# Optimization experiments

Measured on AMD Instinct MI355X. Metric: run time of the kernel, lower is better.

## Reference

```python
import jax, jax.numpy as jnp
import numpy as np

N_GENES = 20000   # num_all_genes
D = 256           # embedding_dim
NNZ = 640000      # nonzeros in GO adjacency (~32 avg degree)
N_COND = 2000     # number of conditions
B = 16384         # batch size
MAXG = 5          # max_genes_per_condition
L = 2             # num_gnn_layers


def setup_inputs() -> dict:
    key = jax.random.key(0)
    ks = jax.random.split(key, 12)
    cond_idx = jax.random.randint(ks[0], (B,), 0, N_COND, dtype=jnp.int32)
    pert_embedding = jax.random.normal(ks[1], (N_GENES, D), jnp.float32) * 0.05
    gnn_kernels = jax.random.normal(ks[2], (L, D, D), jnp.float32) * 0.05
    mlp_w1 = jax.random.normal(ks[3], (D, D), jnp.float32) * 0.05
    mlp_b1 = jnp.zeros((D,), jnp.float32)
    mlp_w2 = jax.random.normal(ks[4], (D, D), jnp.float32) * 0.05
    mlp_b2 = jnp.zeros((D,), jnp.float32)
    adj_row = jax.random.randint(ks[5], (NNZ,), 0, N_GENES, dtype=jnp.int64)
    adj_col = jax.random.randint(ks[6], (NNZ,), 0, N_GENES, dtype=jnp.int64)
    adj_vals = jax.random.uniform(ks[7], (NNZ,), jnp.float32)
    cond_gene_idx = jax.random.randint(ks[8], (N_COND, MAXG), 0, N_GENES, dtype=jnp.int32)
    counts = jax.random.randint(ks[9], (N_COND,), 0, MAXG + 1)
    cond_gene_mask = (jnp.arange(MAXG)[None, :] < counts[:, None]).astype(jnp.float32)
    # padded slots get -1 index like the original (later clamped to 0)
    cond_gene_idx = jnp.where(cond_gene_mask > 0, cond_gene_idx, -1)
    return {
        'cond_idx': cond_idx,
        'pert_embedding': pert_embedding,
        'gnn_kernels': gnn_kernels,
        'mlp_w1': mlp_w1, 'mlp_b1': mlp_b1,
        'mlp_w2': mlp_w2, 'mlp_b2': mlp_b2,
        'adj_row': adj_row, 'adj_col': adj_col, 'adj_vals': adj_vals,
        'cond_gene_idx': cond_gene_idx, 'cond_gene_mask': cond_gene_mask,
    }


def reference(cond_idx, pert_embedding, gnn_kernels, mlp_w1, mlp_b1,
              mlp_w2, mlp_b2, adj_row, adj_col, adj_vals,
              cond_gene_idx, cond_gene_mask):
    # --- GNN over the full gene graph (sparse adjacency @ dense emb, then dense kernel) ---
    emb = pert_embedding  # [N, D]
    for i in range(L):
        # SpMM: aggregated[r] = sum_{nnz with row r} vals * emb[col]
        msgs = adj_vals[:, None] * emb[adj_col]            # [NNZ, D]
        agg = jax.ops.segment_sum(msgs, adj_row, num_segments=N_GENES)  # [N, D]
        emb = agg @ gnn_kernels[i]                          # [N, D]
        if i < L - 1:
            emb = jax.nn.relu(emb)

    # --- per-condition gather of up to MAXG gene embeddings, masked sum ---
    gidx = cond_gene_idx[cond_idx]          # [B, MAXG] int
    gmask = cond_gene_mask[cond_idx]        # [B, MAXG]
    gidx_safe = jnp.maximum(gidx, 0)
    gene_embs = emb[gidx_safe]              # [B, MAXG, D]
    summed = jnp.sum(gene_embs * gmask[:, :, None], axis=1)  # [B, D]
    n_genes = jnp.sum(gmask, axis=1)        # [B]

    # --- small MLP (applied when n_genes > 1), identity when ==1, zeros when ==0 ---
    h = jax.nn.relu(summed @ mlp_w1 + mlp_b1)
    mlp_out = jax.nn.relu(h @ mlp_w2 + mlp_b2)  # [B, D]

    n = n_genes[:, None]
    out = jnp.where(n == 0.0, 0.0, jnp.where(n == 1.0, summed, mlp_out))
    return out
```

## Files before the change

### kernel.cpp

```cpp
#include <hip/hip_runtime.h>

static constexpr int N_GENES = 20000;
static constexpr int D       = 256;
static constexpr int NNZ     = 640000;
static constexpr int BATCH   = 16384;
static constexpr int MAXG    = 5;
static constexpr int SCAN_B  = (N_GENES + 255) / 256;

using bf16x8 = __attribute__((ext_vector_type(8))) short;
using f32x4  = __attribute__((ext_vector_type(4))) float;

__device__ __forceinline__ unsigned short f2bf(float f) {
  unsigned int u = __builtin_bit_cast(unsigned int, f);
  u += 0x7fffu + ((u >> 16) & 1u);
  return (unsigned short)(u >> 16);
}
__device__ __forceinline__ float bf2f(unsigned short h) {
  unsigned int u = ((unsigned int)h) << 16;
  return __builtin_bit_cast(float, u);
}
__device__ __forceinline__ void gload16(const void* g, void* l) {
  __builtin_amdgcn_global_load_lds(
      (const __attribute__((address_space(1))) unsigned int*)g,
      (__attribute__((address_space(3))) unsigned int*)l, 16, 0, 0);
}

__global__ void zero_int(int* __restrict__ p, int n) {
  int i = blockIdx.x * blockDim.x + threadIdx.x;
  if (i < n) p[i] = 0;
}

__global__ void count_rows(const int* __restrict__ adj_row, int* __restrict__ cnt) {
  int e = blockIdx.x * blockDim.x + threadIdx.x;
  if (e < NNZ) atomicAdd(&cnt[adj_row[e]], 1);
}

__global__ __launch_bounds__(256)
void scan_partial(const int* __restrict__ cnt, int* __restrict__ bsum) {
  __shared__ int red[256];
  int b = blockIdx.x, t = threadIdx.x, i = b * 256 + t;
  red[t] = (i < N_GENES) ? cnt[i] : 0;
  __syncthreads();
  for (int off = 128; off > 0; off >>= 1) {
    if (t < off) red[t] += red[t + off];
    __syncthreads();
  }
  if (t == 0) bsum[b] = red[0];
}

__global__ __launch_bounds__(128)
void scan_bsums(const int* __restrict__ bsum, int* __restrict__ bpre,
                int* __restrict__ total_out) {
  __shared__ int s[128];
  int t = threadIdx.x;
  int x = (t < SCAN_B) ? bsum[t] : 0;
  s[t] = x;
  __syncthreads();
  for (int off = 1; off < 128; off <<= 1) {
    int v = (t >= off) ? s[t - off] : 0;
    __syncthreads();
    s[t] += v;
    __syncthreads();
  }
  if (t < SCAN_B) bpre[t] = s[t] - x;
  if (t == SCAN_B - 1) total_out[0] = s[t];
}

__global__ __launch_bounds__(256)
void scan_final(const int* __restrict__ cnt, const int* __restrict__ bpre,
                int* __restrict__ row_ptr, int* __restrict__ fill_ctr) {
  __shared__ int s[256];
  int b = blockIdx.x, t = threadIdx.x, i = b * 256 + t;
  int x = (i < N_GENES) ? cnt[i] : 0;
  s[t] = x;
  __syncthreads();
  for (int off = 1; off < 256; off <<= 1) {
    int v = (t >= off) ? s[t - off] : 0;
    __syncthreads();
    s[t] += v;
    __syncthreads();
  }
  if (i < N_GENES) {
    int e = bpre[b] + s[t] - x;
    row_ptr[i] = e;
    fill_ctr[i] = e;
  }
}

__global__ void fill_csr(const int* __restrict__ adj_row,
                         const int* __restrict__ adj_col,
                         const float* __restrict__ vals,
                         int* __restrict__ fill_ctr, unsigned int* __restrict__ edges) {
  int e = blockIdx.x * blockDim.x + threadIdx.x;
  if (e < NNZ) {
    int r = adj_row[e];
    int p = atomicAdd(&fill_ctr[r], 1);
    edges[p] = (unsigned int)adj_col[e] | ((unsigned int)f2bf(vals[e]) << 16);
  }
}

__global__ __launch_bounds__(256)
void conv_pert(const float* __restrict__ p, ushort4* __restrict__ o) {
  int i = blockIdx.x * 256 + threadIdx.x;
  float4 v = reinterpret_cast<const float4*>(p)[i];
  ushort4 r;
  r.x = f2bf(v.x); r.y = f2bf(v.y); r.z = f2bf(v.z); r.w = f2bf(v.w);
  o[i] = r;
}

__global__ void conv_weights(const float* __restrict__ gk, const float* __restrict__ w1,
                             const float* __restrict__ w2,
                             char* __restrict__ whi, char* __restrict__ wlo) {
  int g = blockIdx.x * 256 + threadIdx.x;
  int wid = g >> 13, rest = g & 8191;
  const float* W = (wid == 0) ? gk : (wid == 1) ? gk + 65536 : (wid == 2) ? w1 : w2;
  int c  = rest >> 9;
  int nc = c >> 2, kt = c & 3;
  int o  = (rest & 511) << 4;
  int n  = o >> 7;
  int wb = (o & 127) ^ ((n & 7) << 4);
  int k  = wb >> 1;
  size_t obase = ((size_t)wid << 17) + ((size_t)c << 13) + o;
  unsigned short* ph = (unsigned short*)(whi + obase);
  unsigned short* pl = (unsigned short*)(wlo + obase);
  #pragma unroll
  for (int e = 0; e < 8; ++e) {
    float f = W[(size_t)(kt * 64 + k + e) * 256 + nc * 64 + n];
    unsigned short h = f2bf(f);
    ph[e] = h;
    pl[e] = f2bf(f - bf2f(h));
  }
}

__global__ __launch_bounds__(256)
void spmm_csr_img(const int* __restrict__ row_ptr, const unsigned int* __restrict__ edges,
                  const unsigned short* __restrict__ src,
                  char* __restrict__ hi_img, char* __restrict__ lo_img) {
  int row = blockIdx.x * 4 + (threadIdx.x >> 6);
  int lane = threadIdx.x & 63;
  int beg = row_ptr[row], end = row_ptr[row + 1];
  const unsigned short* sp = src + lane * 4;
  float4 acc = {0.f, 0.f, 0.f, 0.f};
  int j = beg;
  for (; j + 8 <= end; j += 8) {
    unsigned int e0 = edges[j],     e1 = edges[j + 1], e2 = edges[j + 2], e3 = edges[j + 3];
    unsigned int e4 = edges[j + 4], e5 = edges[j + 5], e6 = edges[j + 6], e7 = edges[j + 7];
    ushort4 g0 = *reinterpret_cast<const ushort4*>(sp + (size_t)(e0 & 0xFFFFu) * D);
    ushort4 g1 = *reinterpret_cast<const ushort4*>(sp + (size_t)(e1 & 0xFFFFu) * D);
    ushort4 g2 = *reinterpret_cast<const ushort4*>(sp + (size_t)(e2 & 0xFFFFu) * D);
    ushort4 g3 = *reinterpret_cast<const ushort4*>(sp + (size_t)(e3 & 0xFFFFu) * D);
    ushort4 g4 = *reinterpret_cast<const ushort4*>(sp + (size_t)(e4 & 0xFFFFu) * D);
    ushort4 g5 = *reinterpret_cast<const ushort4*>(sp + (size_t)(e5 & 0xFFFFu) * D);
    ushort4 g6 = *reinterpret_cast<const ushort4*>(sp + (size_t)(e6 & 0xFFFFu) * D);
    ushort4 g7 = *reinterpret_cast<const ushort4*>(sp + (size_t)(e7 & 0xFFFFu) * D);
    float v0 = bf2f(e0 >> 16), v1 = bf2f(e1 >> 16), v2 = bf2f(e2 >> 16), v3 = bf2f(e3 >> 16);
    float v4 = bf2f(e4 >> 16), v5 = bf2f(e5 >> 16), v6 = bf2f(e6 >> 16), v7 = bf2f(e7 >> 16);
    acc.x += v0 * bf2f(g0.x); acc.y += v0 * bf2f(g0.y); acc.z += v0 * bf2f(g0.z); acc.w += v0 * bf2f(g0.w);
    acc.x += v1 * bf2f(g1.x); acc.y += v1 * bf2f(g1.y); acc.z += v1 * bf2f(g1.z); acc.w += v1 * bf2f(g1.w);
    acc.x += v2 * bf2f(g2.x); acc.y += v2 * bf2f(g2.y); acc.z += v2 * bf2f(g2.z); acc.w += v2 * bf2f(g2.w);
    acc.x += v3 * bf2f(g3.x); acc.y += v3 * bf2f(g3.y); acc.z += v3 * bf2f(g3.z); acc.w += v3 * bf2f(g3.w);
    acc.x += v4 * bf2f(g4.x); acc.y += v4 * bf2f(g4.y); acc.z += v4 * bf2f(g4.z); acc.w += v4 * bf2f(g4.w);
    acc.x += v5 * bf2f(g5.x); acc.y += v5 * bf2f(g5.y); acc.z += v5 * bf2f(g5.z); acc.w += v5 * bf2f(g5.w);
    acc.x += v6 * bf2f(g6.x); acc.y += v6 * bf2f(g6.y); acc.z += v6 * bf2f(g6.z); acc.w += v6 * bf2f(g6.w);
    acc.x += v7 * bf2f(g7.x); acc.y += v7 * bf2f(g7.y); acc.z += v7 * bf2f(g7.z); acc.w += v7 * bf2f(g7.w);
  }
  for (; j < end; ++j) {
    unsigned int e = edges[j];
    ushort4 g = *reinterpret_cast<const ushort4*>(sp + (size_t)(e & 0xFFFFu) * D);
    float v = bf2f(e >> 16);
    acc.x += v * bf2f(g.x); acc.y += v * bf2f(g.y); acc.z += v * bf2f(g.z); acc.w += v * bf2f(g.w);
  }
  int mt = row >> 7, r = row & 127, kt = lane >> 4;
  int wb = ((lane & 15) << 3) ^ ((r & 7) << 4);
  size_t off = ((size_t)(mt * 4 + kt) << 14) + (size_t)r * 128 + wb;
  float a4[4] = {acc.x, acc.y, acc.z, acc.w};
  ushort4 hi, lo;
  unsigned short* ph = (unsigned short*)&hi;
  unsigned short* pl = (unsigned short*)&lo;
  #pragma unroll
  for (int e = 0; e < 4; ++e) {
    unsigned short h = f2bf(a4[e]);
    ph[e] = h;
    pl[e] = f2bf(a4[e] - bf2f(h));
  }
  *reinterpret_cast<ushort4*>(hi_img + off) = hi;
  *reinterpret_cast<ushort4*>(lo_img + off) = lo;
}

__global__ __launch_bounds__(256)
void gather_conditions(const int* __restrict__ cond_idx, const int* __restrict__ cg_idx,
                       const float* __restrict__ cg_mask, const float* __restrict__ emb,
                       float* __restrict__ out, char* __restrict__ hi_img,
                       char* __restrict__ lo_img, float* __restrict__ ngenes) {
  int b = blockIdx.x * 4 + (threadIdx.x >> 6);
  int lane = threadIdx.x & 63;
  int c = cond_idx[b];
  float4 acc = {0.f, 0.f, 0.f, 0.f};
  float n = 0.f;
  #pragma unroll
  for (int g = 0; g < MAXG; ++g) {
    float m = cg_mask[c * MAXG + g];
    n += m;
    if (m > 0.f) {
      int gi = cg_idx[c * MAXG + g];
      float4 e = *reinterpret_cast<const float4*>(emb + (size_t)gi * D + lane * 4);
      acc.x += m * e.x; acc.y += m * e.y; acc.z += m * e.z; acc.w += m * e.w;
    }
  }
  *reinterpret_cast<float4*>(out + (size_t)b * D + lane * 4) = acc;
  int mt = b >> 7, r = b & 127, kt = lane >> 4;
  int wb = ((lane & 15) << 3) ^ ((r & 7) << 4);
  size_t off = ((size_t)(mt * 4 + kt) << 14) + (size_t)r * 128 + wb;
  float a4[4] = {acc.x, acc.y, acc.z, acc.w};
  ushort4 hi, lo;
  unsigned short* ph = (unsigned short*)&hi;
  unsigned short* pl = (unsigned short*)&lo;
  #pragma unroll
  for (int e = 0; e < 4; ++e) {
    unsigned short h = f2bf(a4[e]);
    ph[e] = h;
    pl[e] = f2bf(a4[e] - bf2f(h));
  }
  *reinterpret_cast<ushort4*>(hi_img + off) = hi;
  *reinterpret_cast<ushort4*>(lo_img + off) = lo;
  if (lane == 0) ngenes[b] = n;
}

enum Epi { E_F32, E_RELU_BF16, E_HIMG, E_SELECT };

template <Epi EP>
__global__ __launch_bounds__(256)
void gemm_bf16x3(const char* __restrict__ Ahi, const char* __restrict__ Alo,
                 const char* __restrict__ Bhi, const char* __restrict__ Blo,
                 const float* __restrict__ bias, float* __restrict__ C,
                 unsigned short* __restrict__ Cbf,
                 char* __restrict__ Ohi, char* __restrict__ Olo,
                 const float* __restrict__ ngenes, int M) {
  __shared__ __align__(16) char smem[65536];
  char* sAh = smem;
  char* sAl = smem + 16384;
  char* sBh = smem + 32768;
  char* sBl = smem + 49152;

  const int t   = threadIdx.x;
  const int w   = t >> 6, l = t & 63;
  const int wr  = w >> 1, wc = w & 1;
  const int mt  = blockIdx.y, nt2 = blockIdx.x;

  f32x4 acc[4][4] = {};

  const int rA = l & 15;
  const int kB = (l >> 4) << 4;
  const int xA = (rA & 7) << 4;

  for (int kt = 0; kt < 4; ++kt) {
    const char* gAh  = Ahi + ((size_t)(mt * 4 + kt) << 14);
    const char* gAl  = Alo + ((size_t)(mt * 4 + kt) << 14);
    const char* gBh0 = Bhi + ((size_t)((nt2 * 2 + 0) * 4 + kt) << 13);
    const char* gBl0 = Blo + ((size_t)((nt2 * 2 + 0) * 4 + kt) << 13);
    const char* gBh1 = Bhi + ((size_t)((nt2 * 2 + 1) * 4 + kt) << 13);
    const char* gBl1 = Blo + ((size_t)((nt2 * 2 + 1) * 4 + kt) << 13);
    #pragma unroll
    for (int j = 0; j < 4; ++j) {
      gload16(gAh + (j * 256 + t) * 16, sAh + j * 4096 + w * 1024);
      gload16(gAl + (j * 256 + t) * 16, sAl + j * 4096 + w * 1024);
    }
    #pragma unroll
    for (int j = 0; j < 2; ++j) {
      gload16(gBh0 + (j * 256 + t) * 16, sBh + j * 4096 + w * 1024);
      gload16(gBl0 + (j * 256 + t) * 16, sBl + j * 4096 + w * 1024);
    }
    #pragma unroll
    for (int j = 0; j < 2; ++j) {
      gload16(gBh1 + (j * 256 + t) * 16, sBh + 8192 + j * 4096 + w * 1024);
      gload16(gBl1 + (j * 256 + t) * 16, sBl + 8192 + j * 4096 + w * 1024);
    }
    asm volatile("s_waitcnt vmcnt(0)" ::: "memory");
    __syncthreads();
    #pragma unroll
    for (int ks = 0; ks < 2; ++ks) {
      bf16x8 ah[4], al[4], bh[4], bl[4];
      #pragma unroll
      for (int i = 0; i < 4; ++i) {
        int r   = wr * 64 + i * 16 + rA;
        int off = r * 128 + ((ks * 64 + kB) ^ xA);
        ah[i] = *(const bf16x8*)(sAh + off);
        al[i] = *(const bf16x8*)(sAl + off);
      }
      #pragma unroll
      for (int j = 0; j < 4; ++j) {
        int n   = wc * 64 + j * 16 + rA;
        int off = n * 128 + ((ks * 64 + kB) ^ xA);
        bh[j] = *(const bf16x8*)(sBh + off);
        bl[j] = *(const bf16x8*)(sBl + off);
      }
      #pragma unroll
      for (int i = 0; i < 4; ++i)
        #pragma unroll
        for (int j = 0; j < 4; ++j) {
          acc[i][j] = __builtin_amdgcn_mfma_f32_16x16x32_bf16(ah[i], bh[j], acc[i][j], 0, 0, 0);
          acc[i][j] = __builtin_amdgcn_mfma_f32_16x16x32_bf16(ah[i], bl[j], acc[i][j], 0, 0, 0);
          acc[i][j] = __builtin_amdgcn_mfma_f32_16x16x32_bf16(al[i], bh[j], acc[i][j], 0, 0, 0);
        }
    }
    __syncthreads();
  }

  const int cr = (l >> 4) << 2;
  const int cc = l & 15;
  #pragma unroll
  for (int i = 0; i < 4; ++i) {
    #pragma unroll
    for (int rr = 0; rr < 4; ++rr) {
      int rin  = wr * 64 + i * 16 + cr + rr;
      int grow = mt * 128 + rin;
      if (grow >= M) continue;
      bool wr_row = true;
      if (EP == E_SELECT) wr_row = (ngenes[grow] >= 1.5f);
      #pragma unroll
      for (int j = 0; j < 4; ++j) {
        float v    = acc[i][j][rr];
        int colin  = wc * 64 + j * 16 + cc;
        int gcol   = nt2 * 128 + colin;
        if (EP == E_HIMG || EP == E_SELECT) v += bias[gcol];
        if (EP != E_F32) v = fmaxf(v, 0.f);
        if (EP == E_HIMG) {
          int kt2 = nt2 * 2 + (colin >> 6);
          int k2  = colin & 63;
          int wb  = (k2 << 1) ^ ((rin & 7) << 4);
          size_t off = ((size_t)(mt * 4 + kt2) << 14) + (size_t)rin * 128 + wb;
          unsigned short h16 = f2bf(v);
          *(unsigned short*)(Ohi + off) = h16;
          *(unsigned short*)(Olo + off) = f2bf(v - bf2f(h16));
        } else if (EP == E_RELU_BF16) {
          Cbf[(size_t)grow * 256 + gcol] = f2bf(v);
        } else if (wr_row) {
          C[(size_t)grow * 256 + gcol] = v;
        }
      }
    }
  }
}

extern "C" void kernel_launch(void* const* d_in, const int* in_sizes, int n_in,
                              void* d_out, int out_size, void* d_ws, size_t ws_size,
                              hipStream_t stream) {
  const int*   cond_idx = (const int*)d_in[0];
  const float* pert     = (const float*)d_in[1];
  const float* gnn_k    = (const float*)d_in[2];
  const float* w1       = (const float*)d_in[3];
  const float* b1       = (const float*)d_in[4];
  const float* w2       = (const float*)d_in[5];
  const float* b2       = (const float*)d_in[6];
  const int*   adj_row  = (const int*)d_in[7];
  const int*   adj_col  = (const int*)d_in[8];
  const float* adj_vals = (const float*)d_in[9];
  const int*   cg_idx   = (const int*)d_in[10];
  const float* cg_mask  = (const float*)d_in[11];
  float* out = (float*)d_out;

  char* w = (char*)d_ws;
  auto alloc = [&](size_t bytes) {
    void* p = w;
    w += (bytes + 255) & ~size_t(255);
    return p;
  };
  constexpr int MT_G = (N_GENES + 127) / 128;
  constexpr int MT_B = BATCH / 128;
  char*         aggHi   = (char*)alloc((size_t)MT_G * 4 * 16384);
  char*         aggLo   = (char*)alloc((size_t)MT_G * 4 * 16384);
  float*        embf    = (float*)alloc((size_t)N_GENES * D * 4);
  char*         sumHi   = (char*)alloc((size_t)MT_B * 4 * 16384);
  char*         sumLo   = (char*)alloc((size_t)MT_B * 4 * 16384);
  char*         hHi     = (char*)alloc((size_t)MT_B * 4 * 16384);
  char*         hLo     = (char*)alloc((size_t)MT_B * 4 * 16384);
  char*         wHi     = (char*)alloc((size_t)4 << 17);
  char*         wLo     = (char*)alloc((size_t)4 << 17);
  unsigned int* edges   = (unsigned int*)alloc((size_t)NNZ * 4);
  int*          cnt     = (int*)alloc((size_t)N_GENES * 4);
  int*          row_ptr = (int*)alloc((size_t)(N_GENES + 4) * 4);
  int*          fill_ctr= (int*)alloc((size_t)N_GENES * 4);
  int*          bsum    = (int*)alloc((size_t)128 * 4);
  int*          bpre    = (int*)alloc((size_t)128 * 4);
  float*        ngenes  = (float*)alloc((size_t)BATCH * 4);

  unsigned short* pert_bf = (unsigned short*)hHi;
  unsigned short* embf_bf = (unsigned short*)embf;

  zero_int<<<(N_GENES + 255) / 256, 256, 0, stream>>>(cnt, N_GENES);
  count_rows<<<NNZ / 256, 256, 0, stream>>>(adj_row, cnt);
  scan_partial<<<SCAN_B, 256, 0, stream>>>(cnt, bsum);
  scan_bsums<<<1, 128, 0, stream>>>(bsum, bpre, row_ptr + N_GENES);
  scan_final<<<SCAN_B, 256, 0, stream>>>(cnt, bpre, row_ptr, fill_ctr);
  fill_csr<<<NNZ / 256, 256, 0, stream>>>(adj_row, adj_col, adj_vals, fill_ctr, edges);

  conv_weights<<<128, 256, 0, stream>>>(gnn_k, w1, w2, wHi, wLo);
  conv_pert<<<N_GENES * D / 4 / 256, 256, 0, stream>>>(pert, (ushort4*)pert_bf);

  spmm_csr_img<<<N_GENES / 4, 256, 0, stream>>>(row_ptr, edges, pert_bf, aggHi, aggLo);
  gemm_bf16x3<E_RELU_BF16><<<dim3(2, MT_G), 256, 0, stream>>>(
      aggHi, aggLo, wHi, wLo, nullptr, nullptr, embf_bf, nullptr, nullptr, nullptr, N_GENES);

  spmm_csr_img<<<N_GENES / 4, 256, 0, stream>>>(row_ptr, edges, embf_bf, aggHi, aggLo);
  gemm_bf16x3<E_F32><<<dim3(2, MT_G), 256, 0, stream>>>(
      aggHi, aggLo, wHi + (1 << 17), wLo + (1 << 17), nullptr, embf, nullptr, nullptr, nullptr, nullptr, N_GENES);

  gather_conditions<<<BATCH / 4, 256, 0, stream>>>(cond_idx, cg_idx, cg_mask, embf,
                                                   out, sumHi, sumLo, ngenes);

  gemm_bf16x3<E_HIMG><<<dim3(2, MT_B), 256, 0, stream>>>(
      sumHi, sumLo, wHi + (2 << 17), wLo + (2 << 17), b1, nullptr, nullptr, hHi, hLo, nullptr, BATCH);

  gemm_bf16x3<E_SELECT><<<dim3(2, MT_B), 256, 0, stream>>>(
      hHi, hLo, wHi + (3 << 17), wLo + (3 << 17), b2, out, nullptr, nullptr, nullptr, ngenes, BATCH);
}
```

Measured before the change: 329.9 us.

## Fuse CSR fill and conversion kernels, merge block-sum scan, remap GEMM blocks per XCD

The single-block scan of block sums is folded into the final scan kernel, with each block recomputing the prefix redundantly. The CSR edge fill, weight conversion and embedding bf16 conversion are merged into one launch using block-range dispatch. GEMM launches switch to a 1D grid whose block index is remapped so that consecutive tiles land on the same XCD, aiming at better L2 reuse of the shared B weights and A tiles. Together these cut three kernel launches and change the cache locality of the GEMMs.

```diff
diff --git a/kernel.cpp b/kernel.cpp
--- a/kernel.cpp
+++ b/kernel.cpp
@@ -48,29 +48,21 @@
   if (t == 0) bsum[b] = red[0];
 }
 
-__global__ __launch_bounds__(128)
-void scan_bsums(const int* __restrict__ bsum, int* __restrict__ bpre,
-                int* __restrict__ total_out) {
-  __shared__ int s[128];
-  int t = threadIdx.x;
-  int x = (t < SCAN_B) ? bsum[t] : 0;
-  s[t] = x;
+__global__ __launch_bounds__(256)
+void scan_final2(const int* __restrict__ cnt, const int* __restrict__ bsum,
+                 int* __restrict__ row_ptr, int* __restrict__ fill_ctr) {
+  __shared__ int bs[128];
+  __shared__ int s[256];
+  int b = blockIdx.x, t = threadIdx.x, i = b * 256 + t;
+  if (t < 128) bs[t] = (t < SCAN_B) ? bsum[t] : 0;
   __syncthreads();
   for (int off = 1; off < 128; off <<= 1) {
-    int v = (t >= off) ? s[t - off] : 0;
-    __syncthreads();
-    s[t] += v;
-    __syncthreads();
-  }
-  if (t < SCAN_B) bpre[t] = s[t] - x;
-  if (t == SCAN_B - 1) total_out[0] = s[t];
-}
-
-__global__ __launch_bounds__(256)
-void scan_final(const int* __restrict__ cnt, const int* __restrict__ bpre,
-                int* __restrict__ row_ptr, int* __restrict__ fill_ctr) {
-  __shared__ int s[256];
-  int b = blockIdx.x, t = threadIdx.x, i = b * 256 + t;
+    int v = (t >= off && t < 128) ? bs[t - off] : 0;
+    __syncthreads();
+    if (t < 128) bs[t] += v;
+    __syncthreads();
+  }
+  int bpre = (b == 0) ? 0 : bs[b - 1];
   int x = (i < N_GENES) ? cnt[i] : 0;
   s[t] = x;
   __syncthreads();
@@ -81,54 +73,53 @@
     __syncthreads();
   }
   if (i < N_GENES) {
-    int e = bpre[b] + s[t] - x;
+    int e = bpre + s[t] - x;
     row_ptr[i] = e;
     fill_ctr[i] = e;
   }
-}
-
-__global__ void fill_csr(const int* __restrict__ adj_row,
-                         const int* __restrict__ adj_col,
-                         const float* __restrict__ vals,
-                         int* __restrict__ fill_ctr, unsigned int* __restrict__ edges) {
-  int e = blockIdx.x * blockDim.x + threadIdx.x;
-  if (e < NNZ) {
+  if (b == 0 && t == 0) row_ptr[N_GENES] = NNZ;
+}
+
+__global__ __launch_bounds__(256)
+void fused_fill_conv(const int* __restrict__ adj_row, const int* __restrict__ adj_col,
+                     const float* __restrict__ vals, int* __restrict__ fill_ctr,
+                     unsigned int* __restrict__ edges,
+                     const float* __restrict__ gk, const float* __restrict__ w1,
+                     const float* __restrict__ w2,
+                     char* __restrict__ whi, char* __restrict__ wlo,
+                     const float* __restrict__ pert, ushort4* __restrict__ pert_bf) {
+  int b = blockIdx.x, t = threadIdx.x;
+  if (b < 2500) {
+    int e = b * 256 + t;
     int r = adj_row[e];
     int p = atomicAdd(&fill_ctr[r], 1);
     edges[p] = (unsigned int)adj_col[e] | ((unsigned int)f2bf(vals[e]) << 16);
-  }
-}
-
-__global__ __launch_bounds__(256)
-void conv_pert(const float* __restrict__ p, ushort4* __restrict__ o) {
-  int i = blockIdx.x * 256 + threadIdx.x;
-  float4 v = reinterpret_cast<const float4*>(p)[i];
-  ushort4 r;
-  r.x = f2bf(v.x); r.y = f2bf(v.y); r.z = f2bf(v.z); r.w = f2bf(v.w);
-  o[i] = r;
-}
-
-__global__ void conv_weights(const float* __restrict__ gk, const float* __restrict__ w1,
-                             const float* __restrict__ w2,
-                             char* __restrict__ whi, char* __restrict__ wlo) {
-  int g = blockIdx.x * 256 + threadIdx.x;
-  int wid = g >> 13, rest = g & 8191;
-  const float* W = (wid == 0) ? gk : (wid == 1) ? gk + 65536 : (wid == 2) ? w1 : w2;
-  int c  = rest >> 9;
-  int nc = c >> 2, kt = c & 3;
-  int o  = (rest & 511) << 4;
-  int n  = o >> 7;
-  int wb = (o & 127) ^ ((n & 7) << 4);
-  int k  = wb >> 1;
-  size_t obase = ((size_t)wid << 17) + ((size_t)c << 13) + o;
-  unsigned short* ph = (unsigned short*)(whi + obase);
-  unsigned short* pl = (unsigned short*)(wlo + obase);
-  #pragma unroll
-  for (int e = 0; e < 8; ++e) {
-    float f = W[(size_t)(kt * 64 + k + e) * 256 + nc * 64 + n];
-    unsigned short h = f2bf(f);
-    ph[e] = h;
-    pl[e] = f2bf(f - bf2f(h));
+  } else if (b < 2628) {
+    int g = (b - 2500) * 256 + t;
+    int wid = g >> 13, rest = g & 8191;
+    const float* W = (wid == 0) ? gk : (wid == 1) ? gk + 65536 : (wid == 2) ? w1 : w2;
+    int c  = rest >> 9;
+    int nc = c >> 2, kt = c & 3;
+    int o  = (rest & 511) << 4;
+    int n  = o >> 7;
+    int wb = (o & 127) ^ ((n & 7) << 4);
+    int k  = wb >> 1;
+    size_t obase = ((size_t)wid << 17) + ((size_t)c << 13) + o;
+    unsigned short* ph = (unsigned short*)(whi + obase);
+    unsigned short* pl = (unsigned short*)(wlo + obase);
+    #pragma unroll
+    for (int e2 = 0; e2 < 8; ++e2) {
+      float f = W[(size_t)(kt * 64 + k + e2) * 256 + nc * 64 + n];
+      unsigned short h = f2bf(f);
+      ph[e2] = h;
+      pl[e2] = f2bf(f - bf2f(h));
+    }
+  } else {
+    int i = (b - 2628) * 256 + t;
+    float4 v = reinterpret_cast<const float4*>(pert)[i];
+    ushort4 r4;
+    r4.x = f2bf(v.x); r4.y = f2bf(v.y); r4.z = f2bf(v.z); r4.w = f2bf(v.w);
+    pert_bf[i] = r4;
   }
 }
 
@@ -242,10 +233,16 @@
   char* sBh = smem + 32768;
   char* sBl = smem + 49152;
 
-  const int t   = threadIdx.x;
-  const int w   = t >> 6, l = t & 63;
-  const int wr  = w >> 1, wc = w & 1;
-  const int mt  = blockIdx.y, nt2 = blockIdx.x;
+  const int t = threadIdx.x;
+  const int w = t >> 6, l = t & 63;
+  const int wr = w >> 1, wc = w & 1;
+
+  const int nwg  = gridDim.x;
+  const int orig = blockIdx.x;
+  const int xcd = orig & 7, boff = orig >> 3;
+  const int q = nwg >> 3, r8 = nwg & 7;
+  const int wgid = (xcd < r8 ? xcd * (q + 1) : r8 * (q + 1) + (xcd - r8) * q) + boff;
+  const int mt = wgid >> 1, nt2 = wgid & 1;
 
   f32x4 acc[4][4] = {};
 
@@ -381,7 +378,6 @@
   int*          row_ptr = (int*)alloc((size_t)(N_GENES + 4) * 4);
   int*          fill_ctr= (int*)alloc((size_t)N_GENES * 4);
   int*          bsum    = (int*)alloc((size_t)128 * 4);
-  int*          bpre    = (int*)alloc((size_t)128 * 4);
   float*        ngenes  = (float*)alloc((size_t)BATCH * 4);
 
   unsigned short* pert_bf = (unsigned short*)hHi;
@@ -390,27 +386,25 @@
   zero_int<<<(N_GENES + 255) / 256, 256, 0, stream>>>(cnt, N_GENES);
   count_rows<<<NNZ / 256, 256, 0, stream>>>(adj_row, cnt);
   scan_partial<<<SCAN_B, 256, 0, stream>>>(cnt, bsum);
-  scan_bsums<<<1, 128, 0, stream>>>(bsum, bpre, row_ptr + N_GENES);
-  scan_final<<<SCAN_B, 256, 0, stream>>>(cnt, bpre, row_ptr, fill_ctr);
-  fill_csr<<<NNZ / 256, 256, 0, stream>>>(adj_row, adj_col, adj_vals, fill_ctr, edges);
-
-  conv_weights<<<128, 256, 0, stream>>>(gnn_k, w1, w2, wHi, wLo);
-  conv_pert<<<N_GENES * D / 4 / 256, 256, 0, stream>>>(pert, (ushort4*)pert_bf);
+  scan_final2<<<SCAN_B, 256, 0, stream>>>(cnt, bsum, row_ptr, fill_ctr);
+  fused_fill_conv<<<2500 + 128 + 5000, 256, 0, stream>>>(
+      adj_row, adj_col, adj_vals, fill_ctr, edges,
+      gnn_k, w1, w2, wHi, wLo, pert, (ushort4*)pert_bf);
 
   spmm_csr_img<<<N_GENES / 4, 256, 0, stream>>>(row_ptr, edges, pert_bf, aggHi, aggLo);
-  gemm_bf16x3<E_RELU_BF16><<<dim3(2, MT_G), 256, 0, stream>>>(
+  gemm_bf16x3<E_RELU_BF16><<<2 * MT_G, 256, 0, stream>>>(
       aggHi, aggLo, wHi, wLo, nullptr, nullptr, embf_bf, nullptr, nullptr, nullptr, N_GENES);
 
   spmm_csr_img<<<N_GENES / 4, 256, 0, stream>>>(row_ptr, edges, embf_bf, aggHi, aggLo);
-  gemm_bf16x3<E_F32><<<dim3(2, MT_G), 256, 0, stream>>>(
+  gemm_bf16x3<E_F32><<<2 * MT_G, 256, 0, stream>>>(
       aggHi, aggLo, wHi + (1 << 17), wLo + (1 << 17), nullptr, embf, nullptr, nullptr, nullptr, nullptr, N_GENES);
 
   gather_conditions<<<BATCH / 4, 256, 0, stream>>>(cond_idx, cg_idx, cg_mask, embf,
                                                    out, sumHi, sumLo, ngenes);
 
-  gemm_bf16x3<E_HIMG><<<dim3(2, MT_B), 256, 0, stream>>>(
+  gemm_bf16x3<E_HIMG><<<2 * MT_B, 256, 0, stream>>>(
       sumHi, sumLo, wHi + (2 << 17), wLo + (2 << 17), b1, nullptr, nullptr, hHi, hLo, nullptr, BATCH);
 
-  gemm_bf16x3<E_SELECT><<<dim3(2, MT_B), 256, 0, stream>>>(
+  gemm_bf16x3<E_SELECT><<<2 * MT_B, 256, 0, stream>>>(
       hHi, hLo, wHi + (3 << 17), wLo + (3 << 17), b2, out, nullptr, nullptr, nullptr, ngenes, BATCH);
 }
```

Result: faster. 314.6 us (-4.6%).
